# Optimization experiments

Hardware: AMD Instinct MI355X
Metric: run time of the kernel (lower is better)

The kernel has to match this reference:

```python
import jax, jax.numpy as jnp
import numpy as np

N_NODES = 50000
N_EDGES = 800000
N_FEAT = 128
HIDDEN = 64
N_GRAPHS = 256


def setup_inputs() -> dict:
    key = jax.random.key(0)
    ks = jax.random.split(key, 10)
    x = jax.random.normal(ks[0], (N_NODES, N_FEAT), dtype=jnp.float32)
    edge_index = jax.random.randint(ks[1], (2, N_EDGES), 0, N_NODES, dtype=jnp.int64)
    batch = jnp.sort(jax.random.randint(ks[2], (N_NODES,), 0, N_GRAPHS, dtype=jnp.int64))
    s1 = 1.0 / np.sqrt(N_FEAT)
    s2 = 1.0 / np.sqrt(HIDDEN)
    W1 = jax.random.normal(ks[3], (N_FEAT, HIDDEN), dtype=jnp.float32) * s1
    b1 = jnp.zeros((HIDDEN,), dtype=jnp.float32)
    W2 = jax.random.normal(ks[4], (HIDDEN, HIDDEN), dtype=jnp.float32) * s2
    b2 = jnp.zeros((HIDDEN,), dtype=jnp.float32)
    Wm1 = jax.random.normal(ks[5], (HIDDEN, HIDDEN), dtype=jnp.float32) * s2
    bm1 = jnp.zeros((HIDDEN,), dtype=jnp.float32)
    Wm2 = jax.random.normal(ks[6], (HIDDEN, 1), dtype=jnp.float32) * s2
    bm2 = jnp.zeros((1,), dtype=jnp.float32)
    return {"x": x, "edge_index": edge_index, "batch": batch,
            "W1": W1, "b1": b1, "W2": W2, "b2": b2,
            "Wm1": Wm1, "bm1": bm1, "Wm2": Wm2, "bm2": bm2}


def _gcn_layer(h, W, b, src, dst, norm, n_nodes):
    # GCNConv: h @ W, then symmetric-normalized scatter-add over edges (+ self-loops), + bias
    h = h @ W
    msg = h[src] * norm[:, None]              # [E+N, H] gather + scale
    agg = jax.ops.segment_sum(msg, dst, num_segments=n_nodes)
    return agg + b


def reference(x, edge_index, batch, W1, b1, W2, b2, Wm1, bm1, Wm2, bm2):
    n = x.shape[0]
    loops = jnp.arange(n, dtype=edge_index.dtype)
    src = jnp.concatenate([edge_index[0], loops])  # self-loops as in PyG GCNConv
    dst = jnp.concatenate([edge_index[1], loops])
    deg = jax.ops.segment_sum(jnp.ones_like(dst, dtype=x.dtype), dst, num_segments=n)
    dis = jnp.where(deg > 0, jax.lax.rsqrt(deg), 0.0)  # deg^-1/2
    norm = dis[src] * dis[dst]

    h = jax.nn.relu(_gcn_layer(x, W1, b1, src, dst, norm, n))
    h = jax.nn.relu(_gcn_layer(h, W2, b2, src, dst, norm, n))

    # global mean pool over graphs
    sums = jax.ops.segment_sum(h, batch, num_segments=N_GRAPHS)
    cnts = jax.ops.segment_sum(jnp.ones((n,), dtype=h.dtype), batch, num_segments=N_GRAPHS)
    pooled = sums / jnp.maximum(cnts, 1.0)[:, None]

    # MLP head (dropout inactive at eval)
    out = jax.nn.relu(pooled @ Wm1 + bm1) @ Wm2 + bm2
    return out.reshape(-1)
```

## Files before the change

kernel.cpp:

```cpp
#include <hip/hip_runtime.h>

#define NN 50000
#define NE 800000
#define NF 128
#define NH 64
#define NG 256
#define NB 196
#define NC 196
#define CH 4096
#define CELL 80
#define CAP 5120

typedef __attribute__((ext_vector_type(8))) short bf16x8;
typedef __attribute__((ext_vector_type(4))) float f32x4;

static __device__ __forceinline__ unsigned short f2bf(float f) {
    union { float f; unsigned u; } v; v.f = f;
    unsigned r = v.u + 0x7FFF + ((v.u >> 16) & 1);
    return (unsigned short)(r >> 16);
}
static __device__ __forceinline__ float lo16(unsigned u) {
    return __uint_as_float(u << 16);
}
static __device__ __forceinline__ float hi16(unsigned u) {
    return __uint_as_float(u & 0xFFFF0000u);
}

__global__ __launch_bounds__(256) void part_scatter(const int* __restrict__ ei,
                                                    int* __restrict__ histg,
                                                    int2* __restrict__ ebuf) {
    const int t = threadIdx.x;
    const int c = blockIdx.x;
    const int c0 = c * CH;
    __shared__ int hist[256];
    __shared__ int incl[256];
    __shared__ int lcur[256];
    __shared__ int2 lpairs[CH];

    hist[t] = 0;
    __syncthreads();

    int2 loc[16];
#pragma unroll
    for (int j = 0; j < 16; ++j) {
        int e = c0 + j * 256 + t;
        int s = -1, d = -1;
        if (e < NE) {
            s = ei[e]; d = ei[NE + e];
            atomicAdd(&hist[d >> 8], 1);
        }
        loc[j] = make_int2(s, d);
    }
    __syncthreads();

    int v = hist[t];
    incl[t] = v;
    __syncthreads();
    for (int off = 1; off < 256; off <<= 1) {
        int u = (t >= off) ? incl[t - off] : 0;
        __syncthreads();
        incl[t] += u;
        __syncthreads();
    }
    lcur[t] = incl[t] - v;
    if (t < NB) histg[c * NB + t] = v;
    __syncthreads();

#pragma unroll
    for (int j = 0; j < 16; ++j) {
        int d = loc[j].y;
        if (d >= 0) {
            int p = atomicAdd(&lcur[d >> 8], 1);
            lpairs[p] = loc[j];
        }
    }
    __syncthreads();

    const int total = incl[255];
    for (int p = t; p < total; p += 256) {
        int2 pr = lpairs[p];
        int b = pr.y >> 8;
        int i = p - (incl[b] - hist[b]);
        ebuf[(b * NC + c) * CELL + i] = pr;
    }
}

__global__ __launch_bounds__(256) void build_csr(const int2* __restrict__ ebuf,
                                                 const int* __restrict__ histg,
                                                 int2* __restrict__ row_range,
                                                 float* __restrict__ dis,
                                                 int* __restrict__ csr_src) {
    const int b = blockIdx.x, t = threadIdx.x;
    const int e0 = b * CAP;
    const int node = b * 256 + t;
    __shared__ int coff[256];
    __shared__ int deg_l[256];
    __shared__ int pre[256];
    __shared__ int cur[256];
    __shared__ int2 lpairs[CAP];
    __shared__ int lsrc[CAP];

    int cv = (t < NB) ? histg[t * NB + b] : 0;
    coff[t] = cv;
    __syncthreads();
    for (int off = 1; off < 256; off <<= 1) {
        int u = (t >= off) ? coff[t - off] : 0;
        __syncthreads();
        coff[t] += u;
        __syncthreads();
    }
    if (cv > 0) {
        const int2* src = &ebuf[(b * NC + t) * CELL];
        int dst = coff[t] - cv;
        for (int i = 0; i < cv; ++i)
            lpairs[dst + i] = src[i];
    }
    deg_l[t] = (node < NN) ? 1 : 0;
    __syncthreads();

    const int total = coff[255];
    for (int i = t; i < total; i += 256)
        atomicAdd(&deg_l[lpairs[i].y & 255], 1);
    __syncthreads();

    int v = deg_l[t];
    pre[t] = v;
    __syncthreads();
    for (int off = 1; off < 256; off <<= 1) {
        int u = (t >= off) ? pre[t - off] : 0;
        __syncthreads();
        pre[t] += u;
        __syncthreads();
    }
    int excl = pre[t] - v;
    cur[t] = 1;
    if (node < NN) {
        lsrc[excl] = node;
        row_range[node] = make_int2(e0 + excl, e0 + pre[t]);
        dis[node] = rsqrtf((float)v);
    }
    __syncthreads();
    for (int i = t; i < total; i += 256) {
        int2 p = lpairs[i];
        int d = p.y & 255;
        int pos = (pre[d] - deg_l[d]) + atomicAdd(&cur[d], 1);
        lsrc[pos] = p.x;
    }
    __syncthreads();
    const int tot_all = pre[255];
    for (int i = t; i < tot_all; i += 256)
        csr_src[e0 + i] = lsrc[i];
}

__global__ __launch_bounds__(256) void gemm1_mfma(const float* __restrict__ X,
                                                  const float* __restrict__ W,
                                                  const float* __restrict__ dis,
                                                  unsigned short* __restrict__ Y) {
    __shared__ unsigned short Xs[64 * 136];
    __shared__ unsigned int   Wt[64 * 68];
    const int t = threadIdx.x;
    const int base = blockIdx.x * 64;

    for (int i = t * 4; i < 64 * 128; i += 1024) {
        int node = i >> 7, k = i & 127;
        int gn = base + node; if (gn >= NN) gn = NN - 1;
        float4 v = *(const float4*)&X[(size_t)gn * 128 + k];
        ushort4 o = { f2bf(v.x), f2bf(v.y), f2bf(v.z), f2bf(v.w) };
        *(ushort4*)&Xs[node * 136 + k] = o;
    }
    for (int idx = t; idx < 64 * 64; idx += 256) {
        int n = idx & 63, kp = idx >> 6;
        float w0 = W[(2 * kp) * 64 + n];
        float w1 = W[(2 * kp + 1) * 64 + n];
        Wt[n * 68 + kp] = (unsigned)f2bf(w0) | ((unsigned)f2bf(w1) << 16);
    }
    __syncthreads();

    const int w = t >> 6;
    const int lane = t & 63;
    const int l15 = lane & 15;
    const int quad = lane >> 4;
    f32x4 acc[4] = {{0.f,0.f,0.f,0.f},{0.f,0.f,0.f,0.f},{0.f,0.f,0.f,0.f},{0.f,0.f,0.f,0.f}};
#pragma unroll
    for (int kk = 0; kk < 4; ++kk) {
        const bf16x8 a = *(const bf16x8*)&Xs[(w * 16 + l15) * 136 + quad * 8 + kk * 32];
#pragma unroll
        for (int nt = 0; nt < 4; ++nt) {
            const bf16x8 b = *(const bf16x8*)&Wt[(nt * 16 + l15) * 68 + quad * 4 + kk * 16];
            acc[nt] = __builtin_amdgcn_mfma_f32_16x16x32_bf16(a, b, acc[nt], 0, 0, 0);
        }
    }
    const int r0 = base + w * 16 + quad * 4;
    float4 d4 = *(const float4*)&dis[r0];
    const float dd[4] = { d4.x, d4.y, d4.z, d4.w };
#pragma unroll
    for (int reg = 0; reg < 4; ++reg) {
        const int row = r0 + reg;
        if (row < NN) {
#pragma unroll
            for (int nt = 0; nt < 4; ++nt)
                Y[(size_t)row * 64 + nt * 16 + l15] = f2bf(acc[nt][reg] * dd[reg]);
        }
    }
}

static __device__ __forceinline__ void acc8(float* acc, const uint4 u) {
    acc[0] += lo16(u.x); acc[1] += hi16(u.x);
    acc[2] += lo16(u.y); acc[3] += hi16(u.y);
    acc[4] += lo16(u.z); acc[5] += hi16(u.z);
    acc[6] += lo16(u.w); acc[7] += hi16(u.w);
}

static __device__ __forceinline__ void gather_rows(const unsigned short* __restrict__ h,
                                                   const int* __restrict__ csr_src,
                                                   int lo, int hi, int p8, float* acc) {
    int i = lo;
    for (; i + 4 <= hi; i += 4) {
        const int i0 = csr_src[i];
        const int i1 = csr_src[i + 1];
        const int i2 = csr_src[i + 2];
        const int i3 = csr_src[i + 3];
        const uint4 u0 = *(const uint4*)&h[(i0 << 6) + p8];
        const uint4 u1 = *(const uint4*)&h[(i1 << 6) + p8];
        const uint4 u2 = *(const uint4*)&h[(i2 << 6) + p8];
        const uint4 u3 = *(const uint4*)&h[(i3 << 6) + p8];
        acc8(acc, u0); acc8(acc, u1); acc8(acc, u2); acc8(acc, u3);
    }
    for (; i + 2 <= hi; i += 2) {
        const int i0 = csr_src[i];
        const int i1 = csr_src[i + 1];
        const uint4 u0 = *(const uint4*)&h[(i0 << 6) + p8];
        const uint4 u1 = *(const uint4*)&h[(i1 << 6) + p8];
        acc8(acc, u0); acc8(acc, u1);
    }
    if (i < hi) {
        const int i0 = csr_src[i];
        acc8(acc, *(const uint4*)&h[(i0 << 6) + p8]);
    }
}

__global__ __launch_bounds__(256) void agg_gemv(const unsigned short* __restrict__ h,
                                                const int2* __restrict__ row_range,
                                                const int* __restrict__ csr_src,
                                                const float* __restrict__ dis,
                                                const float* __restrict__ b1,
                                                const float* __restrict__ W2,
                                                unsigned short* __restrict__ g) {
    __shared__ unsigned short W2b[64 * 72];
    __shared__ unsigned short A[32 * 72];
    const int t = threadIdx.x;
    for (int idx = t; idx < 64 * 32; idx += 256) {
        int n = idx & 63, kp = idx >> 6;
        unsigned short w0 = f2bf(W2[(2 * kp) * 64 + n]);
        unsigned short w1 = f2bf(W2[(2 * kp + 1) * 64 + n]);
        *(unsigned*)&W2b[n * 72 + 2 * kp] = (unsigned)w0 | ((unsigned)w1 << 16);
    }

    const int base = blockIdx.x * 32;
    const int nloc = t >> 3;
    const int p8 = (t & 7) * 8;
    const int n = base + nloc;
    float acc[8] = {};
    if (n < NN) {
        const int2 rr = row_range[n];
        gather_rows(h, csr_src, rr.x, rr.y, p8, acc);
        const float dn = dis[n];
        const float4 bv0 = *(const float4*)&b1[p8];
        const float4 bv1 = *(const float4*)&b1[p8 + 4];
        acc[0] = fmaxf(acc[0] * dn + bv0.x, 0.f) * dn;
        acc[1] = fmaxf(acc[1] * dn + bv0.y, 0.f) * dn;
        acc[2] = fmaxf(acc[2] * dn + bv0.z, 0.f) * dn;
        acc[3] = fmaxf(acc[3] * dn + bv0.w, 0.f) * dn;
        acc[4] = fmaxf(acc[4] * dn + bv1.x, 0.f) * dn;
        acc[5] = fmaxf(acc[5] * dn + bv1.y, 0.f) * dn;
        acc[6] = fmaxf(acc[6] * dn + bv1.z, 0.f) * dn;
        acc[7] = fmaxf(acc[7] * dn + bv1.w, 0.f) * dn;
    }
    uint4 pk;
    pk.x = (unsigned)f2bf(acc[0]) | ((unsigned)f2bf(acc[1]) << 16);
    pk.y = (unsigned)f2bf(acc[2]) | ((unsigned)f2bf(acc[3]) << 16);
    pk.z = (unsigned)f2bf(acc[4]) | ((unsigned)f2bf(acc[5]) << 16);
    pk.w = (unsigned)f2bf(acc[6]) | ((unsigned)f2bf(acc[7]) << 16);
    *(uint4*)&A[nloc * 72 + p8] = pk;
    __syncthreads();

    const int w = t >> 6;
    const int lane = t & 63;
    const int l15 = lane & 15;
    const int quad = lane >> 4;
    const int mt = w & 1;
    const int nq = (w >> 1) * 2;
    const bf16x8 a0 = *(const bf16x8*)&A[(mt * 16 + l15) * 72 + quad * 8];
    const bf16x8 a1 = *(const bf16x8*)&A[(mt * 16 + l15) * 72 + 32 + quad * 8];
    const bf16x8 b00 = *(const bf16x8*)&W2b[(nq * 16 + l15) * 72 + quad * 8];
    const bf16x8 b01 = *(const bf16x8*)&W2b[(nq * 16 + l15) * 72 + 32 + quad * 8];
    const bf16x8 b10 = *(const bf16x8*)&W2b[((nq + 1) * 16 + l15) * 72 + quad * 8];
    const bf16x8 b11 = *(const bf16x8*)&W2b[((nq + 1) * 16 + l15) * 72 + 32 + quad * 8];
    f32x4 c0 = {0.f, 0.f, 0.f, 0.f}, c1 = {0.f, 0.f, 0.f, 0.f};
    c0 = __builtin_amdgcn_mfma_f32_16x16x32_bf16(a0, b00, c0, 0, 0, 0);
    c0 = __builtin_amdgcn_mfma_f32_16x16x32_bf16(a1, b01, c0, 0, 0, 0);
    c1 = __builtin_amdgcn_mfma_f32_16x16x32_bf16(a0, b10, c1, 0, 0, 0);
    c1 = __builtin_amdgcn_mfma_f32_16x16x32_bf16(a1, b11, c1, 0, 0, 0);
    const int r0 = base + mt * 16 + quad * 4;
#pragma unroll
    for (int reg = 0; reg < 4; ++reg) {
        const int row = r0 + reg;
        if (row < NN) {
            g[(size_t)row * 64 + nq * 16 + l15] = f2bf(c0[reg]);
            g[(size_t)row * 64 + (nq + 1) * 16 + l15] = f2bf(c1[reg]);
        }
    }
}

__global__ __launch_bounds__(256) void agg_pool(const unsigned short* __restrict__ h,
                                                const int2* __restrict__ row_range,
                                                const int* __restrict__ csr_src,
                                                const float* __restrict__ dis,
                                                const float* __restrict__ bias,
                                                const int* __restrict__ batch,
                                                float* __restrict__ psum) {
    __shared__ float rowsL[32 * 68];
    __shared__ int nb[32];
    const int t = threadIdx.x;
    const int nloc = t >> 3;
    const int n = blockIdx.x * 32 + nloc;
    const int p8 = (t & 7) * 8;
    if ((t & 7) == 0) nb[nloc] = (n < NN) ? batch[n] : -1;
    if (n < NN) {
        const int2 rr = row_range[n];
        float acc[8] = {};
        gather_rows(h, csr_src, rr.x, rr.y, p8, acc);
        const float dn = dis[n];
        const float4 bv0 = *(const float4*)&bias[p8];
        const float4 bv1 = *(const float4*)&bias[p8 + 4];
        float4 r0, r1;
        r0.x = fmaxf(acc[0] * dn + bv0.x, 0.f);
        r0.y = fmaxf(acc[1] * dn + bv0.y, 0.f);
        r0.z = fmaxf(acc[2] * dn + bv0.z, 0.f);
        r0.w = fmaxf(acc[3] * dn + bv0.w, 0.f);
        r1.x = fmaxf(acc[4] * dn + bv1.x, 0.f);
        r1.y = fmaxf(acc[5] * dn + bv1.y, 0.f);
        r1.z = fmaxf(acc[6] * dn + bv1.z, 0.f);
        r1.w = fmaxf(acc[7] * dn + bv1.w, 0.f);
        *(float4*)&rowsL[nloc * 68 + p8] = r0;
        *(float4*)&rowsL[nloc * 68 + p8 + 4] = r1;
    }
    __syncthreads();
    if (t < 64) {
        float s = 0.f; int curg = -2;
        for (int r = 0; r < 32; ++r) {
            const int gg = nb[r];
            if (gg != curg) {
                if (curg >= 0) atomicAdd(&psum[curg * 64 + t], s);
                s = 0.f; curg = gg;
            }
            if (gg >= 0) s += rowsL[r * 68 + t];
        }
        if (curg >= 0) atomicAdd(&psum[curg * 64 + t], s);
    }
}

__global__ __launch_bounds__(64) void head_kernel(const float* __restrict__ psum,
                                                  const int* __restrict__ batch,
                                                  const float* __restrict__ Wm1,
                                                  const float* __restrict__ bm1,
                                                  const float* __restrict__ Wm2,
                                                  const float* __restrict__ bm2,
                                                  float* __restrict__ out) {
    const int g = blockIdx.x;
    const int t = threadIdx.x;
    int lo = 0, hi = NN;
    while (lo < hi) { int m = (lo + hi) >> 1; if (batch[m] < g) lo = m + 1; else hi = m; }
    const int s = lo;
    hi = NN;
    while (lo < hi) { int m = (lo + hi) >> 1; if (batch[m] < g + 1) lo = m + 1; else hi = m; }
    const int cnt = lo - s;

    __shared__ float pl[64];
    pl[t] = psum[g * 64 + t] / (float)(cnt > 0 ? cnt : 1);
    __syncthreads();
    float z = bm1[t];
#pragma unroll 8
    for (int k = 0; k < 64; ++k)
        z += pl[k] * Wm1[k * 64 + t];
    z = fmaxf(z, 0.f);
    float y = z * Wm2[t];
    for (int off = 32; off; off >>= 1) y += __shfl_down(y, off);
    if (t == 0) out[g] = y + bm2[0];
}

extern "C" void kernel_launch(void* const* d_in, const int* in_sizes, int n_in,
                              void* d_out, int out_size, void* d_ws, size_t ws_size,
                              hipStream_t stream) {
    const float* x   = (const float*)d_in[0];
    const int*   ei  = (const int*)d_in[1];
    const int*   bat = (const int*)d_in[2];
    const float* W1  = (const float*)d_in[3];
    const float* b1  = (const float*)d_in[4];
    const float* W2  = (const float*)d_in[5];
    const float* b2  = (const float*)d_in[6];
    const float* Wm1 = (const float*)d_in[7];
    const float* bm1 = (const float*)d_in[8];
    const float* Wm2 = (const float*)d_in[9];
    const float* bm2 = (const float*)d_in[10];
    float* out = (float*)d_out;

    char* w = (char*)d_ws;
    int*            histg     = (int*)           (w + 0);
    int2*           row_range = (int2*)          (w + 153664);
    float*          dis       = (float*)         (w + 553664);
    int*            csr_src   = (int*)           (w + 753664);
    int2*           ebuf      = (int2*)          (w + 4767744);
    unsigned short* bufA      = (unsigned short*)(w + 29353984);
    unsigned short* bufB      = (unsigned short*)(w + 35753984);
    float*          psum      = (float*)         (w + 42153984);

    hipMemsetAsync(psum, 0, NG * NH * sizeof(float), stream);
    part_scatter<<<NC, 256, 0, stream>>>(ei, histg, ebuf);
    build_csr   <<<NB, 256, 0, stream>>>(ebuf, histg, row_range, dis, csr_src);

    gemm1_mfma<<<(NN + 63) / 64, 256, 0, stream>>>(x, W1, dis, bufA);
    agg_gemv  <<<(NN + 31) / 32, 256, 0, stream>>>(bufA, row_range, csr_src, dis, b1, W2, bufB);
    agg_pool  <<<(NN + 31) / 32, 256, 0, stream>>>(bufB, row_range, csr_src, dis, b2, bat, psum);
    head_kernel<<<NG, 64, 0, stream>>>(psum, bat, Wm1, bm1, Wm2, bm2, out);
}
```

Before: 161.3 us.

## Fuse edge partitioning, psum zeroing and first GEMM into one kernel

The first GEMM no longer scales rows by deg^-1/2, so it no longer depends on the CSR build and can run in the same launch as the edge partitioning, as extra blocks. The psum memset also moves into those blocks. To keep the maths the same, both aggregation kernels now look up dis[src] per neighbour and apply it as an FMA weight, and agg_gemv drops the pre-scaling of its output. This removes two launches and lets the GEMM overlap the scatter, but each gathered edge now needs an extra random 4-byte load.

```diff
diff --git a/kernel.cpp b/kernel.cpp
--- a/kernel.cpp
+++ b/kernel.cpp
@@ -10,6 +10,7 @@
 #define CH 4096
 #define CELL 80
 #define CAP 5120
+#define NGB 782
 
 typedef __attribute__((ext_vector_type(8))) short bf16x8;
 typedef __attribute__((ext_vector_type(4))) float f32x4;
@@ -26,62 +27,118 @@
     return __uint_as_float(u & 0xFFFF0000u);
 }
 
-__global__ __launch_bounds__(256) void part_scatter(const int* __restrict__ ei,
-                                                    int* __restrict__ histg,
-                                                    int2* __restrict__ ebuf) {
+__global__ __launch_bounds__(256) void prep_gemm(const int* __restrict__ ei,
+                                                 int* __restrict__ histg,
+                                                 int2* __restrict__ ebuf,
+                                                 const float* __restrict__ X,
+                                                 const float* __restrict__ W,
+                                                 unsigned short* __restrict__ Y,
+                                                 float* __restrict__ psum) {
+    __shared__ __align__(16) char smem[35840];
     const int t = threadIdx.x;
-    const int c = blockIdx.x;
-    const int c0 = c * CH;
-    __shared__ int hist[256];
-    __shared__ int incl[256];
-    __shared__ int lcur[256];
-    __shared__ int2 lpairs[CH];
-
-    hist[t] = 0;
-    __syncthreads();
-
-    int2 loc[16];
-#pragma unroll
-    for (int j = 0; j < 16; ++j) {
-        int e = c0 + j * 256 + t;
-        int s = -1, d = -1;
-        if (e < NE) {
-            s = ei[e]; d = ei[NE + e];
-            atomicAdd(&hist[d >> 8], 1);
-        }
-        loc[j] = make_int2(s, d);
-    }
-    __syncthreads();
-
-    int v = hist[t];
-    incl[t] = v;
-    __syncthreads();
-    for (int off = 1; off < 256; off <<= 1) {
-        int u = (t >= off) ? incl[t - off] : 0;
-        __syncthreads();
-        incl[t] += u;
-        __syncthreads();
-    }
-    lcur[t] = incl[t] - v;
-    if (t < NB) histg[c * NB + t] = v;
-    __syncthreads();
-
-#pragma unroll
-    for (int j = 0; j < 16; ++j) {
-        int d = loc[j].y;
-        if (d >= 0) {
-            int p = atomicAdd(&lcur[d >> 8], 1);
-            lpairs[p] = loc[j];
-        }
-    }
-    __syncthreads();
-
-    const int total = incl[255];
-    for (int p = t; p < total; p += 256) {
-        int2 pr = lpairs[p];
-        int b = pr.y >> 8;
-        int i = p - (incl[b] - hist[b]);
-        ebuf[(b * NC + c) * CELL + i] = pr;
+
+    if (blockIdx.x < NC) {
+        int* hist = (int*)smem;
+        int* incl = hist + 256;
+        int* lcur = incl + 256;
+        int2* lpairs = (int2*)(smem + 3072);
+        const int c = blockIdx.x;
+        const int c0 = c * CH;
+
+        hist[t] = 0;
+        __syncthreads();
+
+        int2 loc[16];
+#pragma unroll
+        for (int j = 0; j < 16; ++j) {
+            int e = c0 + j * 256 + t;
+            int s = -1, d = -1;
+            if (e < NE) {
+                s = ei[e]; d = ei[NE + e];
+                atomicAdd(&hist[d >> 8], 1);
+            }
+            loc[j] = make_int2(s, d);
+        }
+        __syncthreads();
+
+        int v = hist[t];
+        incl[t] = v;
+        __syncthreads();
+        for (int off = 1; off < 256; off <<= 1) {
+            int u = (t >= off) ? incl[t - off] : 0;
+            __syncthreads();
+            incl[t] += u;
+            __syncthreads();
+        }
+        lcur[t] = incl[t] - v;
+        if (t < NB) histg[c * NB + t] = v;
+        __syncthreads();
+
+#pragma unroll
+        for (int j = 0; j < 16; ++j) {
+            int d = loc[j].y;
+            if (d >= 0) {
+                int p = atomicAdd(&lcur[d >> 8], 1);
+                lpairs[p] = loc[j];
+            }
+        }
+        __syncthreads();
+
+        const int total = incl[255];
+        for (int p = t; p < total; p += 256) {
+            int2 pr = lpairs[p];
+            int b = pr.y >> 8;
+            int i = p - (incl[b] - hist[b]);
+            ebuf[(b * NC + c) * CELL + i] = pr;
+        }
+    } else {
+        const int gb = blockIdx.x - NC;
+        if (gb < 16)
+            *(float4*)&psum[gb * 1024 + t * 4] = make_float4(0.f, 0.f, 0.f, 0.f);
+
+        unsigned short* Xs = (unsigned short*)smem;
+        unsigned int* Wt = (unsigned int*)(smem + 17408);
+        const int base = gb * 64;
+
+        for (int i = t * 4; i < 64 * 128; i += 1024) {
+            int node = i >> 7, k = i & 127;
+            int gn = base + node; if (gn >= NN) gn = NN - 1;
+            float4 v = *(const float4*)&X[(size_t)gn * 128 + k];
+            ushort4 o = { f2bf(v.x), f2bf(v.y), f2bf(v.z), f2bf(v.w) };
+            *(ushort4*)&Xs[node * 136 + k] = o;
+        }
+        for (int idx = t; idx < 64 * 64; idx += 256) {
+            int n = idx & 63, kp = idx >> 6;
+            float w0 = W[(2 * kp) * 64 + n];
+            float w1 = W[(2 * kp + 1) * 64 + n];
+            Wt[n * 68 + kp] = (unsigned)f2bf(w0) | ((unsigned)f2bf(w1) << 16);
+        }
+        __syncthreads();
+
+        const int w = t >> 6;
+        const int lane = t & 63;
+        const int l15 = lane & 15;
+        const int quad = lane >> 4;
+        f32x4 acc[4] = {{0.f,0.f,0.f,0.f},{0.f,0.f,0.f,0.f},{0.f,0.f,0.f,0.f},{0.f,0.f,0.f,0.f}};
+#pragma unroll
+        for (int kk = 0; kk < 4; ++kk) {
+            const bf16x8 a = *(const bf16x8*)&Xs[(w * 16 + l15) * 136 + quad * 8 + kk * 32];
+#pragma unroll
+            for (int nt = 0; nt < 4; ++nt) {
+                const bf16x8 b = *(const bf16x8*)&Wt[(nt * 16 + l15) * 68 + quad * 4 + kk * 16];
+                acc[nt] = __builtin_amdgcn_mfma_f32_16x16x32_bf16(a, b, acc[nt], 0, 0, 0);
+            }
+        }
+        const int r0 = base + w * 16 + quad * 4;
+#pragma unroll
+        for (int reg = 0; reg < 4; ++reg) {
+            const int row = r0 + reg;
+            if (row < NN) {
+#pragma unroll
+                for (int nt = 0; nt < 4; ++nt)
+                    Y[(size_t)row * 64 + nt * 16 + l15] = f2bf(acc[nt][reg]);
+            }
+        }
     }
 }
 
@@ -152,90 +209,42 @@
         csr_src[e0 + i] = lsrc[i];
 }
 
-__global__ __launch_bounds__(256) void gemm1_mfma(const float* __restrict__ X,
-                                                  const float* __restrict__ W,
-                                                  const float* __restrict__ dis,
-                                                  unsigned short* __restrict__ Y) {
-    __shared__ unsigned short Xs[64 * 136];
-    __shared__ unsigned int   Wt[64 * 68];
-    const int t = threadIdx.x;
-    const int base = blockIdx.x * 64;
-
-    for (int i = t * 4; i < 64 * 128; i += 1024) {
-        int node = i >> 7, k = i & 127;
-        int gn = base + node; if (gn >= NN) gn = NN - 1;
-        float4 v = *(const float4*)&X[(size_t)gn * 128 + k];
-        ushort4 o = { f2bf(v.x), f2bf(v.y), f2bf(v.z), f2bf(v.w) };
-        *(ushort4*)&Xs[node * 136 + k] = o;
-    }
-    for (int idx = t; idx < 64 * 64; idx += 256) {
-        int n = idx & 63, kp = idx >> 6;
-        float w0 = W[(2 * kp) * 64 + n];
-        float w1 = W[(2 * kp + 1) * 64 + n];
-        Wt[n * 68 + kp] = (unsigned)f2bf(w0) | ((unsigned)f2bf(w1) << 16);
-    }
-    __syncthreads();
-
-    const int w = t >> 6;
-    const int lane = t & 63;
-    const int l15 = lane & 15;
-    const int quad = lane >> 4;
-    f32x4 acc[4] = {{0.f,0.f,0.f,0.f},{0.f,0.f,0.f,0.f},{0.f,0.f,0.f,0.f},{0.f,0.f,0.f,0.f}};
-#pragma unroll
-    for (int kk = 0; kk < 4; ++kk) {
-        const bf16x8 a = *(const bf16x8*)&Xs[(w * 16 + l15) * 136 + quad * 8 + kk * 32];
-#pragma unroll
-        for (int nt = 0; nt < 4; ++nt) {
-            const bf16x8 b = *(const bf16x8*)&Wt[(nt * 16 + l15) * 68 + quad * 4 + kk * 16];
-            acc[nt] = __builtin_amdgcn_mfma_f32_16x16x32_bf16(a, b, acc[nt], 0, 0, 0);
-        }
-    }
-    const int r0 = base + w * 16 + quad * 4;
-    float4 d4 = *(const float4*)&dis[r0];
-    const float dd[4] = { d4.x, d4.y, d4.z, d4.w };
-#pragma unroll
-    for (int reg = 0; reg < 4; ++reg) {
-        const int row = r0 + reg;
-        if (row < NN) {
-#pragma unroll
-            for (int nt = 0; nt < 4; ++nt)
-                Y[(size_t)row * 64 + nt * 16 + l15] = f2bf(acc[nt][reg] * dd[reg]);
-        }
-    }
-}
-
-static __device__ __forceinline__ void acc8(float* acc, const uint4 u) {
-    acc[0] += lo16(u.x); acc[1] += hi16(u.x);
-    acc[2] += lo16(u.y); acc[3] += hi16(u.y);
-    acc[4] += lo16(u.z); acc[5] += hi16(u.z);
-    acc[6] += lo16(u.w); acc[7] += hi16(u.w);
-}
-
-static __device__ __forceinline__ void gather_rows(const unsigned short* __restrict__ h,
-                                                   const int* __restrict__ csr_src,
-                                                   int lo, int hi, int p8, float* acc) {
+static __device__ __forceinline__ void acc8w(float* acc, const uint4 u, float w) {
+    acc[0] = fmaf(w, lo16(u.x), acc[0]); acc[1] = fmaf(w, hi16(u.x), acc[1]);
+    acc[2] = fmaf(w, lo16(u.y), acc[2]); acc[3] = fmaf(w, hi16(u.y), acc[3]);
+    acc[4] = fmaf(w, lo16(u.z), acc[4]); acc[5] = fmaf(w, hi16(u.z), acc[5]);
+    acc[6] = fmaf(w, lo16(u.w), acc[6]); acc[7] = fmaf(w, hi16(u.w), acc[7]);
+}
+
+static __device__ __forceinline__ void gather_rows_w(const unsigned short* __restrict__ h,
+                                                     const int* __restrict__ csr_src,
+                                                     const float* __restrict__ dis,
+                                                     int lo, int hi, int p8, float* acc) {
     int i = lo;
     for (; i + 4 <= hi; i += 4) {
         const int i0 = csr_src[i];
         const int i1 = csr_src[i + 1];
         const int i2 = csr_src[i + 2];
         const int i3 = csr_src[i + 3];
+        const float w0 = dis[i0], w1 = dis[i1], w2 = dis[i2], w3 = dis[i3];
         const uint4 u0 = *(const uint4*)&h[(i0 << 6) + p8];
         const uint4 u1 = *(const uint4*)&h[(i1 << 6) + p8];
         const uint4 u2 = *(const uint4*)&h[(i2 << 6) + p8];
         const uint4 u3 = *(const uint4*)&h[(i3 << 6) + p8];
-        acc8(acc, u0); acc8(acc, u1); acc8(acc, u2); acc8(acc, u3);
+        acc8w(acc, u0, w0); acc8w(acc, u1, w1);
+        acc8w(acc, u2, w2); acc8w(acc, u3, w3);
     }
     for (; i + 2 <= hi; i += 2) {
         const int i0 = csr_src[i];
         const int i1 = csr_src[i + 1];
+        const float w0 = dis[i0], w1 = dis[i1];
         const uint4 u0 = *(const uint4*)&h[(i0 << 6) + p8];
         const uint4 u1 = *(const uint4*)&h[(i1 << 6) + p8];
-        acc8(acc, u0); acc8(acc, u1);
+        acc8w(acc, u0, w0); acc8w(acc, u1, w1);
     }
     if (i < hi) {
         const int i0 = csr_src[i];
-        acc8(acc, *(const uint4*)&h[(i0 << 6) + p8]);
+        acc8w(acc, *(const uint4*)&h[(i0 << 6) + p8], dis[i0]);
     }
 }
 
@@ -263,18 +272,18 @@
     float acc[8] = {};
     if (n < NN) {
         const int2 rr = row_range[n];
-        gather_rows(h, csr_src, rr.x, rr.y, p8, acc);
+        gather_rows_w(h, csr_src, dis, rr.x, rr.y, p8, acc);
         const float dn = dis[n];
         const float4 bv0 = *(const float4*)&b1[p8];
         const float4 bv1 = *(const float4*)&b1[p8 + 4];
-        acc[0] = fmaxf(acc[0] * dn + bv0.x, 0.f) * dn;
-        acc[1] = fmaxf(acc[1] * dn + bv0.y, 0.f) * dn;
-        acc[2] = fmaxf(acc[2] * dn + bv0.z, 0.f) * dn;
-        acc[3] = fmaxf(acc[3] * dn + bv0.w, 0.f) * dn;
-        acc[4] = fmaxf(acc[4] * dn + bv1.x, 0.f) * dn;
-        acc[5] = fmaxf(acc[5] * dn + bv1.y, 0.f) * dn;
-        acc[6] = fmaxf(acc[6] * dn + bv1.z, 0.f) * dn;
-        acc[7] = fmaxf(acc[7] * dn + bv1.w, 0.f) * dn;
+        acc[0] = fmaxf(acc[0] * dn + bv0.x, 0.f);
+        acc[1] = fmaxf(acc[1] * dn + bv0.y, 0.f);
+        acc[2] = fmaxf(acc[2] * dn + bv0.z, 0.f);
+        acc[3] = fmaxf(acc[3] * dn + bv0.w, 0.f);
+        acc[4] = fmaxf(acc[4] * dn + bv1.x, 0.f);
+        acc[5] = fmaxf(acc[5] * dn + bv1.y, 0.f);
+        acc[6] = fmaxf(acc[6] * dn + bv1.z, 0.f);
+        acc[7] = fmaxf(acc[7] * dn + bv1.w, 0.f);
     }
     uint4 pk;
     pk.x = (unsigned)f2bf(acc[0]) | ((unsigned)f2bf(acc[1]) << 16);
@@ -329,7 +338,7 @@
     if (n < NN) {
         const int2 rr = row_range[n];
         float acc[8] = {};
-        gather_rows(h, csr_src, rr.x, rr.y, p8, acc);
+        gather_rows_w(h, csr_src, dis, rr.x, rr.y, p8, acc);
         const float dn = dis[n];
         const float4 bv0 = *(const float4*)&bias[p8];
         const float4 bv1 = *(const float4*)&bias[p8 + 4];
@@ -415,11 +424,8 @@
     unsigned short* bufB      = (unsigned short*)(w + 35753984);
     float*          psum      = (float*)         (w + 42153984);
 
-    hipMemsetAsync(psum, 0, NG * NH * sizeof(float), stream);
-    part_scatter<<<NC, 256, 0, stream>>>(ei, histg, ebuf);
-    build_csr   <<<NB, 256, 0, stream>>>(ebuf, histg, row_range, dis, csr_src);
-
-    gemm1_mfma<<<(NN + 63) / 64, 256, 0, stream>>>(x, W1, dis, bufA);
+    prep_gemm <<<NC + NGB, 256, 0, stream>>>(ei, histg, ebuf, x, W1, bufA, psum);
+    build_csr <<<NB, 256, 0, stream>>>(ebuf, histg, row_range, dis, csr_src);
     agg_gemv  <<<(NN + 31) / 32, 256, 0, stream>>>(bufA, row_range, csr_src, dis, b1, W2, bufB);
     agg_pool  <<<(NN + 31) / 32, 256, 0, stream>>>(bufB, row_range, csr_src, dis, b2, bat, psum);
     head_kernel<<<NG, 64, 0, stream>>>(psum, bat, Wm1, bm1, Wm2, bm2, out);
```

Result: no change. 159.3 us (-1.3%).
